# Kernel tuning notes

Hardware: AMD Instinct MI355X
Metric: run time of the kernel (lower is better)

## Reference

```python
import jax, jax.numpy as jnp
import numpy as np
import math

B, E, H, HD, P, G, N, L, FF = 16, 768, 12, 64, 16, 14, 196, 12, 3072
SQRT_E = math.sqrt(E)
SQRT_HD = math.sqrt(HD)


def cosine_norm(x):
    n = jnp.linalg.norm(x, axis=-1, keepdims=True)
    return x / jnp.maximum(n, 1e-6)


def layer_norm(x, w, b, eps=1e-6):
    m = jnp.mean(x, axis=-1, keepdims=True)
    v = jnp.var(x, axis=-1, keepdims=True)
    return (x - m) / jnp.sqrt(v + eps) * w + b


def setup_inputs() -> dict:
    key = jax.random.key(0)
    ks = jax.random.split(key, 16)
    std = 0.02
    return {
        "x": jax.random.normal(ks[0], (B, 3, 224, 224), jnp.float32),
        "patch_w": jax.random.normal(ks[1], (E, 3, P, P), jnp.float32) * std,
        "patch_b": jnp.zeros((E,), jnp.float32),
        "cls_token": jax.random.normal(ks[2], (1, 1, E), jnp.float32) * std,
        "pos_embed": jax.random.normal(ks[3], (1, N + 1, E), jnp.float32) * std,
        "Wq": jax.random.normal(ks[4], (L, E, E), jnp.float32) * std,
        "Wk": jax.random.normal(ks[5], (L, E, E), jnp.float32) * std,
        "Wv": jax.random.normal(ks[6], (L, E, E), jnp.float32) * std,
        "Wo": jax.random.normal(ks[7], (L, E, E), jnp.float32) * std,
        # Scale params stored at their torch init values (s = ones * scale)
        "s_qk": jnp.ones((L, H, HD), jnp.float32) / SQRT_E,        # scale=1/sqrt(dim)
        "Wup": jax.random.normal(ks[8], (L, FF, E), jnp.float32) * std,
        "Wgate": jax.random.normal(ks[9], (L, FF, E), jnp.float32) * std,
        "Wdown": jax.random.normal(ks[10], (L, E, FF), jnp.float32) * std,
        "s_u": jnp.ones((L, FF), jnp.float32),
        "s_v": jnp.ones((L, FF), jnp.float32),
        "alpha_A": jnp.ones((L, E), jnp.float32) / SQRT_E,         # scale=1/sqrt(dim)
        "alpha_M": jnp.ones((L, E), jnp.float32) / SQRT_E,
        "fc_w": jnp.ones((E,), jnp.float32),
        "fc_b": jnp.zeros((E,), jnp.float32),
    }


def _attention(h, wq, wk, wv, wo, s_qk):
    b, n, _ = h.shape
    q = (h @ wq.T).reshape(b, n, H, HD)
    k = (h @ wk.T).reshape(b, n, H, HD)
    v = (h @ wv.T).reshape(b, n, H, HD)
    # Scale.forward(): s * (init/scale) with init=1, scale=1/sqrt(E)
    s = s_qk * SQRT_E                                   # [H, HD]
    q = cosine_norm(q) * s
    k = cosine_norm(k) * s
    logits = jnp.einsum("bnhd,bmhd->bhnm", q, k) * SQRT_HD
    attn = jax.nn.softmax(logits, axis=-1)
    out = jnp.einsum("bhnm,bmhd->bnhd", attn, v).reshape(b, n, E)
    return out @ wo.T


def _mlp(h, wup, wgate, wdown, s_u, s_v):
    u = (h @ wup.T) * s_u
    v = (h @ wgate.T) * s_v * SQRT_E                    # mlp scale = sqrt(in_features)
    hidden = u * jax.nn.silu(v)
    return hidden @ wdown.T


def _block(h, wq, wk, wv, wo, s_qk, wup, wgate, wdown, s_u, s_v, a_A, a_M):
    # alpha Scale: init=0.05, scale=1/sqrt(E) -> effective = s * 0.05 * sqrt(E)
    aA = a_A * (0.05 * SQRT_E)
    aM = a_M * (0.05 * SQRT_E)
    h_A = cosine_norm(_attention(h, wq, wk, wv, wo, s_qk))
    h = cosine_norm(h + aA * (h_A - h))
    h_M = cosine_norm(_mlp(h, wup, wgate, wdown, s_u, s_v))
    h = cosine_norm(h + aM * (h_M - h))
    return h


def reference(x, patch_w, patch_b, cls_token, pos_embed, Wq, Wk, Wv, Wo, s_qk,
              Wup, Wgate, Wdown, s_u, s_v, alpha_A, alpha_M, fc_w, fc_b):
    b = x.shape[0]
    # patch embed: conv k=stride=16 == patch extraction + linear proj
    patches = x.reshape(b, 3, G, P, G, P).transpose(0, 2, 4, 1, 3, 5).reshape(b, N, 3 * P * P)
    t = patches @ patch_w.reshape(E, -1).T + patch_b    # [B, N, E]
    t = jnp.concatenate([jnp.broadcast_to(cls_token, (b, 1, E)), t], axis=1)
    t = t + pos_embed                                    # [B, N+1, E]
    nodes = None
    for i in range(L):
        t = _block(t, Wq[i], Wk[i], Wv[i], Wo[i], s_qk[i],
                   Wup[i], Wgate[i], Wdown[i], s_u[i], s_v[i], alpha_A[i], alpha_M[i])
        if i == L - 2:
            nodes = layer_norm(t, fc_w, fc_b)[:, 1:]
    edges = layer_norm(t, fc_w, fc_b)[:, 1:]
    return nodes, edges
```

## Files before the change

kernel.cpp:

```cpp
#include <hip/hip_runtime.h>
#include <hip/hip_bf16.h>
#include <cstdint>
#include <cstddef>

typedef __hip_bfloat16 bf16;
typedef short bf16x8 __attribute__((ext_vector_type(8)));
typedef float f32x4 __attribute__((ext_vector_type(4)));

#define SQRT_E   27.712812921102035f
#define ASCALE   (0.05f * 27.712812921102035f)
#define MPAD     3200

__device__ __forceinline__ void load_lds16(const bf16* g, bf16* l) {
    __builtin_amdgcn_global_load_lds(
        (const __attribute__((address_space(1))) void*)g,
        (__attribute__((address_space(3))) void*)l, 16, 0, 0);
}

__device__ __forceinline__ float block_sum(float v, float* sbuf) {
#pragma unroll
    for (int m = 32; m >= 1; m >>= 1) v += __shfl_xor(v, m);
    __syncthreads();
    if ((threadIdx.x & 63) == 0) sbuf[threadIdx.x >> 6] = v;
    __syncthreads();
    return sbuf[0] + sbuf[1] + sbuf[2] + sbuf[3];
}

__device__ __forceinline__ void cvt8(const float* s, bf16* d) {
    float4 f0 = *(const float4*)s;
    float4 f1 = *(const float4*)(s + 4);
    bf16 t[8];
    t[0] = __float2bfloat16(f0.x); t[1] = __float2bfloat16(f0.y);
    t[2] = __float2bfloat16(f0.z); t[3] = __float2bfloat16(f0.w);
    t[4] = __float2bfloat16(f1.x); t[5] = __float2bfloat16(f1.y);
    t[6] = __float2bfloat16(f1.z); t[7] = __float2bfloat16(f1.w);
    *reinterpret_cast<uint4*>(d) = *reinterpret_cast<const uint4*>(t);
}

__device__ __forceinline__ void wconv_body(
    int idx,
    const float* __restrict__ wq, const float* __restrict__ wk,
    const float* __restrict__ wv, const float* __restrict__ wo,
    const float* __restrict__ wu, const float* __restrict__ wg,
    const float* __restrict__ wd, bf16* __restrict__ dst) {
    const float* src;
    size_t off;
    if (idx < 294912) {
        int seg = idx / 73728, o = idx - seg * 73728;
        src = (seg == 0) ? wq : (seg == 1) ? wk : (seg == 2) ? wv : wo;
        off = (size_t)o * 8;
    } else {
        int i2 = idx - 294912;
        int seg = i2 / 294912, o = i2 - seg * 294912;
        src = (seg == 0) ? wu : (seg == 1) ? wg : wd;
        off = (size_t)o * 8;
    }
    cvt8(src + off, dst + (size_t)idx * 8);
}

__global__ __launch_bounds__(256) void prep_kernel(
    const float* __restrict__ x, bf16* __restrict__ A,
    const float* __restrict__ patchw, bf16* __restrict__ pwb,
    const float* __restrict__ wq, const float* __restrict__ wk,
    const float* __restrict__ wv, const float* __restrict__ wo,
    const float* __restrict__ wu, const float* __restrict__ wg,
    const float* __restrict__ wd, bf16* __restrict__ wdst) {
    int b = blockIdx.x, tid = threadIdx.x;
    if (b < 288) {
        int idx = b * 256 + tid;
        cvt8(patchw + (size_t)idx * 8, pwb + (size_t)idx * 8);
    } else if (b < 9888) {
        int idx = (b - 288) * 256 + tid;
        int row = idx / 768, col = idx - row * 768;
        if (row >= 3136) { A[idx] = __float2bfloat16(0.f); return; }
        int bb = row / 196, pp = row - bb * 196;
        int gy = pp / 14, gx = pp - gy * 14;
        int c = col >> 8, rem = col & 255, py = rem >> 4, px = rem & 15;
        A[idx] = __float2bfloat16(
            x[((size_t)(bb * 3 + c) * 224 + gy * 16 + py) * 224 + gx * 16 + px]);
    } else {
        int idx = (b - 9888) * 256 + tid;
        wconv_body(idx, wq, wk, wv, wo, wu, wg, wd, wdst);
    }
}

__global__ __launch_bounds__(256) void assemble_kernel(
    const float* __restrict__ tproj, const float* __restrict__ pb,
    const float* __restrict__ cls, const float* __restrict__ pos,
    float* __restrict__ h, bf16* __restrict__ hb) {
    int row = blockIdx.x;
    int b = row / 197, n = row - b * 197;
#pragma unroll
    for (int i = 0; i < 3; i++) {
        int c = threadIdx.x + i * 256;
        float v;
        if (n == 0) v = cls[c] + pos[c];
        else v = tproj[(size_t)(b * 196 + n - 1) * 768 + c] + pb[c] + pos[(size_t)n * 768 + c];
        h[(size_t)row * 768 + c] = v;
        hb[(size_t)row * 768 + c] = __float2bfloat16(v);
    }
}

__global__ __launch_bounds__(256) void gemm_bt(
    const bf16* __restrict__ A, int lda,
    const bf16* __restrict__ B0, const bf16* __restrict__ B1, const bf16* __restrict__ B2,
    int tilesPerSeg, int segColStride,
    void* __restrict__ Cv, int ldc, long long partStride,
    int Klen, int ldb, int outBf16) {
    __shared__ __align__(16) bf16 As[128 * 32];
    __shared__ __align__(16) bf16 Bs[128 * 32];
    const int tid = threadIdx.x;
    const int lane = tid & 63, wave = tid >> 6;
    const int wm = wave & 1, wn = wave >> 1;
    const int quad = lane >> 4, l16 = lane & 15;
    const int seg = blockIdx.x / tilesPerSeg;
    const int nt = blockIdx.x - seg * tilesPerSeg;
    const bf16* B = (seg == 0) ? B0 : (seg == 1 ? B1 : B2);
    const int row0 = blockIdx.y * 128;
    const int col0 = nt * 128;
    const long long kofs = (long long)blockIdx.z * Klen;
    const bf16* Ab = A + (size_t)row0 * lda + kofs;
    const bf16* Bb = B + (size_t)col0 * ldb + kofs;
    const long long cofs = (long long)blockIdx.z * partStride + (long long)seg * segColStride;

    f32x4 acc[4][4];
    f32x4 zero = {0.f, 0.f, 0.f, 0.f};
#pragma unroll
    for (int i = 0; i < 4; i++)
#pragma unroll
        for (int j = 0; j < 4; j++) acc[i][j] = zero;

    for (int k0 = 0; k0 < Klen; k0 += 32) {
#pragma unroll
        for (int it = 0; it < 2; ++it) {
            int cidx = it * 256 + tid;
            int r = cidx >> 2, cg = cidx & 3;
            load_lds16(Ab + (size_t)r * lda + k0 + cg * 8, As + cidx * 8);
            load_lds16(Bb + (size_t)r * ldb + k0 + cg * 8, Bs + cidx * 8);
        }
        __syncthreads();
        bf16x8 av[4], bv[4];
#pragma unroll
        for (int i = 0; i < 4; i++) {
            av[i] = *(const bf16x8*)(As + (wm * 64 + i * 16 + l16) * 32 + quad * 8);
            bv[i] = *(const bf16x8*)(Bs + (wn * 64 + i * 16 + l16) * 32 + quad * 8);
        }
#pragma unroll
        for (int i = 0; i < 4; i++)
#pragma unroll
            for (int j = 0; j < 4; j++)
                acc[i][j] = __builtin_amdgcn_mfma_f32_16x16x32_bf16(av[i], bv[j], acc[i][j], 0, 0, 0);
        __syncthreads();
    }
    if (outBf16) {
        bf16* Cb = (bf16*)Cv + cofs;
#pragma unroll
        for (int i = 0; i < 4; i++) {
            int rr = row0 + wm * 64 + i * 16 + quad * 4;
#pragma unroll
            for (int j = 0; j < 4; j++) {
                int cc = col0 + wn * 64 + j * 16 + l16;
#pragma unroll
                for (int r = 0; r < 4; r++)
                    Cb[(size_t)(rr + r) * ldc + cc] = __float2bfloat16(acc[i][j][r]);
            }
        }
    } else {
        float* Cb = (float*)Cv + cofs;
#pragma unroll
        for (int i = 0; i < 4; i++) {
            int rr = row0 + wm * 64 + i * 16 + quad * 4;
#pragma unroll
            for (int j = 0; j < 4; j++) {
                int cc = col0 + wn * 64 + j * 16 + l16;
#pragma unroll
                for (int r = 0; r < 4; r++)
                    Cb[(size_t)(rr + r) * ldc + cc] = acc[i][j][r];
            }
        }
    }
}

__global__ __launch_bounds__(256) void oproj_wconv(
    const bf16* __restrict__ A, const bf16* __restrict__ Bw,
    bf16* __restrict__ C, long long partStride,
    const float* __restrict__ wq, const float* __restrict__ wk,
    const float* __restrict__ wv, const float* __restrict__ wo,
    const float* __restrict__ wu, const float* __restrict__ wg,
    const float* __restrict__ wd, bf16* __restrict__ wdst) {
    __shared__ __align__(16) bf16 As[128 * 32];
    __shared__ __align__(16) bf16 Bs[128 * 32];
    const int bb = blockIdx.x;
    const int tid = threadIdx.x;
    if (bb >= 300) {
        int idx = (bb - 300) * 256 + tid;
        wconv_body(idx, wq, wk, wv, wo, wu, wg, wd, wdst);
        return;
    }
    const int lane = tid & 63, wave = tid >> 6;
    const int wm = wave & 1, wn = wave >> 1;
    const int quad = lane >> 4, l16 = lane & 15;
    const int nt = bb % 6;
    const int ry = (bb / 6) % 25;
    const int z  = bb / 150;
    const int row0 = ry * 128, col0 = nt * 128;
    const bf16* Ab = A + (size_t)row0 * 768 + z * 384;
    const bf16* Bb = Bw + (size_t)col0 * 768 + z * 384;

    f32x4 acc[4][4];
    f32x4 zero = {0.f, 0.f, 0.f, 0.f};
#pragma unroll
    for (int i = 0; i < 4; i++)
#pragma unroll
        for (int j = 0; j < 4; j++) acc[i][j] = zero;

    for (int k0 = 0; k0 < 384; k0 += 32) {
#pragma unroll
        for (int it = 0; it < 2; ++it) {
            int cidx = it * 256 + tid;
            int r = cidx >> 2, cg = cidx & 3;
            load_lds16(Ab + (size_t)r * 768 + k0 + cg * 8, As + cidx * 8);
            load_lds16(Bb + (size_t)r * 768 + k0 + cg * 8, Bs + cidx * 8);
        }
        __syncthreads();
        bf16x8 av[4], bv[4];
#pragma unroll
        for (int i = 0; i < 4; i++) {
            av[i] = *(const bf16x8*)(As + (wm * 64 + i * 16 + l16) * 32 + quad * 8);
            bv[i] = *(const bf16x8*)(Bs + (wn * 64 + i * 16 + l16) * 32 + quad * 8);
        }
#pragma unroll
        for (int i = 0; i < 4; i++)
#pragma unroll
            for (int j = 0; j < 4; j++)
                acc[i][j] = __builtin_amdgcn_mfma_f32_16x16x32_bf16(av[i], bv[j], acc[i][j], 0, 0, 0);
        __syncthreads();
    }
    bf16* Cb = C + (long long)z * partStride;
#pragma unroll
    for (int i = 0; i < 4; i++) {
        int rr = row0 + wm * 64 + i * 16 + quad * 4;
#pragma unroll
        for (int j = 0; j < 4; j++) {
            int cc = col0 + wn * 64 + j * 16 + l16;
#pragma unroll
            for (int r = 0; r < 4; r++)
                Cb[(size_t)(rr + r) * 768 + cc] = __float2bfloat16(acc[i][j][r]);
        }
    }
}

__global__ __launch_bounds__(256) void gemm_qkv(
    const bf16* __restrict__ A,
    const bf16* __restrict__ Bq, const bf16* __restrict__ Bk, const bf16* __restrict__ Bv,
    const float* __restrict__ s_l,
    bf16* __restrict__ Qd, bf16* __restrict__ Kd, bf16* __restrict__ VTd) {
    __shared__ __align__(16) bf16 As[128 * 32];
    __shared__ __align__(16) bf16 Bs[128 * 32];
    const int tid = threadIdx.x;
    const int lane = tid & 63, wave = tid >> 6;
    const int wm = wave & 1, wn = wave >> 1;
    const int quad = lane >> 4, l16 = lane & 15;
    const int seg = blockIdx.x / 6;
    const int nt = blockIdx.x - seg * 6;
    const bf16* B = (seg == 0) ? Bq : (seg == 1 ? Bk : Bv);
    const int row0 = blockIdx.y * 128;
    const int col0 = nt * 128;
    const bf16* Ab = A + (size_t)row0 * 768;
    const bf16* Bb = B + (size_t)col0 * 768;

    f32x4 acc[4][4];
    f32x4 zero = {0.f, 0.f, 0.f, 0.f};
#pragma unroll
    for (int i = 0; i < 4; i++)
#pragma unroll
        for (int j = 0; j < 4; j++) acc[i][j] = zero;

    for (int k0 = 0; k0 < 768; k0 += 32) {
#pragma unroll
        for (int it = 0; it < 2; ++it) {
            int cidx = it * 256 + tid;
            int r = cidx >> 2, cg = cidx & 3;
            load_lds16(Ab + (size_t)r * 768 + k0 + cg * 8, As + cidx * 8);
            load_lds16(Bb + (size_t)r * 768 + k0 + cg * 8, Bs + cidx * 8);
        }
        __syncthreads();
        bf16x8 av[4], bv[4];
#pragma unroll
        for (int i = 0; i < 4; i++) {
            av[i] = *(const bf16x8*)(As + (wm * 64 + i * 16 + l16) * 32 + quad * 8);
            bv[i] = *(const bf16x8*)(Bs + (wn * 64 + i * 16 + l16) * 32 + quad * 8);
        }
#pragma unroll
        for (int i = 0; i < 4; i++)
#pragma unroll
            for (int j = 0; j < 4; j++)
                acc[i][j] = __builtin_amdgcn_mfma_f32_16x16x32_bf16(av[i], bv[j], acc[i][j], 0, 0, 0);
        __syncthreads();
    }

    const int hcol = nt * 2 + wn;
    if (seg < 2) {
        bf16* Dst = (seg == 0) ? Qd : Kd;
        float sv0[4];
#pragma unroll
        for (int j = 0; j < 4; j++) sv0[j] = s_l[hcol * 64 + j * 16 + l16] * SQRT_E;
#pragma unroll
        for (int i = 0; i < 4; i++) {
#pragma unroll
            for (int r = 0; r < 4; r++) {
                float ss = acc[i][0][r] * acc[i][0][r] + acc[i][1][r] * acc[i][1][r]
                         + acc[i][2][r] * acc[i][2][r] + acc[i][3][r] * acc[i][3][r];
#pragma unroll
                for (int m = 1; m < 16; m <<= 1) ss += __shfl_xor(ss, m);
                float inv = 1.f / fmaxf(sqrtf(ss), 1e-6f);
                int t = row0 + wm * 64 + i * 16 + quad * 4 + r;
                if (t < 3152) {
                    int b = t / 197, n = t - b * 197;
                    size_t base = ((size_t)(b * 12 + hcol) * 208 + n) * 64;
#pragma unroll
                    for (int j = 0; j < 4; j++)
                        Dst[base + j * 16 + l16] =
                            __float2bfloat16(acc[i][j][r] * inv * sv0[j]);
                }
            }
        }
    } else {
#pragma unroll
        for (int i = 0; i < 4; i++) {
#pragma unroll
            for (int r = 0; r < 4; r++) {
                int t = row0 + wm * 64 + i * 16 + quad * 4 + r;
                if (t < 3152) {
                    int b = t / 197, n = t - b * 197;
                    size_t vbase = (size_t)(b * 12 + hcol) * 64 * 224 + n;
#pragma unroll
                    for (int j = 0; j < 4; j++)
                        VTd[vbase + (size_t)(j * 16 + l16) * 224] =
                            __float2bfloat16(acc[i][j][r]);
                }
            }
        }
    }
}

__global__ __launch_bounds__(256) void gemm_upgate(
    const bf16* __restrict__ A, const bf16* __restrict__ Bu, const bf16* __restrict__ Bv,
    const float* __restrict__ su, const float* __restrict__ sv,
    bf16* __restrict__ H) {
    __shared__ __align__(16) bf16 As[128 * 32];
    __shared__ __align__(16) bf16 Bus[64 * 32];
    __shared__ __align__(16) bf16 Bvs[64 * 32];
    const int tid = threadIdx.x;
    const int lane = tid & 63, wave = tid >> 6;
    const int wm = wave & 1, wn = wave >> 1;
    const int quad = lane >> 4, l16 = lane & 15;
    const int ct = blockIdx.x;
    const int row0 = blockIdx.y * 128;
    const bf16* Ab = A + (size_t)row0 * 768;
    const bf16* Bub = Bu + (size_t)ct * 64 * 768;
    const bf16* Bvb = Bv + (size_t)ct * 64 * 768;

    f32x4 au[4][2], av_[4][2];
    f32x4 zero = {0.f, 0.f, 0.f, 0.f};
#pragma unroll
    for (int i = 0; i < 4; i++)
#pragma unroll
        for (int j = 0; j < 2; j++) { au[i][j] = zero; av_[i][j] = zero; }

    for (int k0 = 0; k0 < 768; k0 += 32) {
#pragma unroll
        for (int it = 0; it < 2; ++it) {
            int cidx = it * 256 + tid;
            int r = cidx >> 2, cg = cidx & 3;
            load_lds16(Ab + (size_t)r * 768 + k0 + cg * 8, As + cidx * 8);
        }
        {
            int r = tid >> 2, cg = tid & 3;
            load_lds16(Bub + (size_t)r * 768 + k0 + cg * 8, Bus + tid * 8);
            load_lds16(Bvb + (size_t)r * 768 + k0 + cg * 8, Bvs + tid * 8);
        }
        __syncthreads();
        bf16x8 a[4], bu[2], bv[2];
#pragma unroll
        for (int i = 0; i < 4; i++)
            a[i] = *(const bf16x8*)(As + (wm * 64 + i * 16 + l16) * 32 + quad * 8);
#pragma unroll
        for (int j = 0; j < 2; j++) {
            bu[j] = *(const bf16x8*)(Bus + (wn * 32 + j * 16 + l16) * 32 + quad * 8);
            bv[j] = *(const bf16x8*)(Bvs + (wn * 32 + j * 16 + l16) * 32 + quad * 8);
        }
#pragma unroll
        for (int i = 0; i < 4; i++)
#pragma unroll
            for (int j = 0; j < 2; j++) {
                au[i][j]  = __builtin_amdgcn_mfma_f32_16x16x32_bf16(a[i], bu[j], au[i][j], 0, 0, 0);
                av_[i][j] = __builtin_amdgcn_mfma_f32_16x16x32_bf16(a[i], bv[j], av_[i][j], 0, 0, 0);
            }
        __syncthreads();
    }
#pragma unroll
    for (int j = 0; j < 2; j++) {
        int cc = ct * 64 + wn * 32 + j * 16 + l16;
        float suc = su[cc];
        float svc = sv[cc] * SQRT_E;
#pragma unroll
        for (int i = 0; i < 4; i++) {
            int rr = row0 + wm * 64 + i * 16 + quad * 4;
#pragma unroll
            for (int r = 0; r < 4; r++) {
                float u = au[i][j][r] * suc;
                float v = av_[i][j][r] * svc;
                float sig = 1.f / (1.f + __expf(-v));
                H[(size_t)(rr + r) * 3072 + cc] = __float2bfloat16(u * v * sig);
            }
        }
    }
}

__global__ __launch_bounds__(64) void attn_kernel(
    const bf16* __restrict__ Q, const bf16* __restrict__ K,
    const bf16* __restrict__ VT, bf16* __restrict__ O) {
    __shared__ __align__(16) bf16 Ps[16 * 224];
    int lane = threadIdx.x;
    int quad = lane >> 4, l16 = lane & 15;
    int bh = blockIdx.x % 192;
    int qt = blockIdx.x / 192;
    int b = bh / 12, h = bh - b * 12;
    const bf16* Qb = Q + (size_t)bh * 208 * 64;
    const bf16* Kb = K + (size_t)bh * 208 * 64;
    const bf16* Vb = VT + (size_t)bh * 64 * 224;
    f32x4 zero = {0.f, 0.f, 0.f, 0.f};

    bf16x8 a0 = *(const bf16x8*)(Qb + (qt * 16 + l16) * 64 + quad * 8);
    bf16x8 a1 = *(const bf16x8*)(Qb + (qt * 16 + l16) * 64 + quad * 8 + 32);

    f32x4 lg[13];
#pragma unroll
    for (int kt = 0; kt < 13; kt++) {
        bf16x8 b0 = *(const bf16x8*)(Kb + (kt * 16 + l16) * 64 + quad * 8);
        bf16x8 b1 = *(const bf16x8*)(Kb + (kt * 16 + l16) * 64 + quad * 8 + 32);
        f32x4 c = zero;
        c = __builtin_amdgcn_mfma_f32_16x16x32_bf16(a0, b0, c, 0, 0, 0);
        c = __builtin_amdgcn_mfma_f32_16x16x32_bf16(a1, b1, c, 0, 0, 0);
        lg[kt] = c;
    }
    float sm[4] = {0.f, 0.f, 0.f, 0.f};
#pragma unroll
    for (int kt = 0; kt < 13; kt++) {
        bool valid = (kt * 16 + l16) < 197;
#pragma unroll
        for (int r = 0; r < 4; r++) {
            float p = valid ? __expf(lg[kt][r] * 8.0f) : 0.f;
            lg[kt][r] = p;
            sm[r] += p;
        }
    }
#pragma unroll
    for (int m = 1; m < 16; m <<= 1)
#pragma unroll
        for (int r = 0; r < 4; r++) sm[r] += __shfl_xor(sm[r], m);
    float inv[4];
#pragma unroll
    for (int r = 0; r < 4; r++) inv[r] = 1.f / sm[r];
#pragma unroll
    for (int kt = 0; kt < 13; kt++)
#pragma unroll
        for (int r = 0; r < 4; r++)
            Ps[(quad * 4 + r) * 224 + kt * 16 + l16] = __float2bfloat16(lg[kt][r]);
#pragma unroll
    for (int r = 0; r < 4; r++)
        Ps[(quad * 4 + r) * 224 + 208 + l16] = __float2bfloat16(0.f);
    __syncthreads();
#pragma unroll
    for (int nt = 0; nt < 4; nt++) {
        f32x4 o = zero;
#pragma unroll
        for (int ks = 0; ks < 7; ks++) {
            bf16x8 pa = *(const bf16x8*)(Ps + l16 * 224 + ks * 32 + quad * 8);
            bf16x8 vb = *(const bf16x8*)(Vb + (nt * 16 + l16) * 224 + ks * 32 + quad * 8);
            o = __builtin_amdgcn_mfma_f32_16x16x32_bf16(pa, vb, o, 0, 0, 0);
        }
#pragma unroll
        for (int r = 0; r < 4; r++) {
            int tok = qt * 16 + quad * 4 + r;
            if (tok < 197)
                O[(size_t)(b * 197 + tok) * 768 + h * 64 + nt * 16 + l16] =
                    __float2bfloat16(o[r] * inv[r]);
        }
    }
}

__global__ __launch_bounds__(256) void residual_cos(
    const bf16* __restrict__ proj, int nParts, long long partStride,
    const float* __restrict__ alpha,
    float* __restrict__ h, bf16* __restrict__ hb,
    const float* __restrict__ fcw, const float* __restrict__ fcb,
    float* __restrict__ lnout) {
    __shared__ float sbuf[4];
    int row = blockIdx.x, tid = threadIdx.x;
    float p[3];
    float ss = 0.f;
#pragma unroll
    for (int i = 0; i < 3; i++) {
        int c = tid + i * 256;
        float v = 0.f;
        for (int pt = 0; pt < nParts; pt++)
            v += __bfloat162float(proj[(long long)pt * partStride + (size_t)row * 768 + c]);
        p[i] = v;
        ss += v * v;
    }
    ss = block_sum(ss, sbuf);
    float inv1 = 1.f / fmaxf(sqrtf(ss), 1e-6f);
    float ss2 = 0.f;
#pragma unroll
    for (int i = 0; i < 3; i++) {
        int c = tid + i * 256;
        float hv = h[(size_t)row * 768 + c];
        float a = alpha[c] * ASCALE;
        float m = hv + a * (p[i] * inv1 - hv);
        p[i] = m;
        ss2 += m * m;
    }
    ss2 = block_sum(ss2, sbuf);
    float inv2 = 1.f / fmaxf(sqrtf(ss2), 1e-6f);
    float v0 = p[0] * inv2, v1 = p[1] * inv2, v2 = p[2] * inv2;
    {
        int c = tid;
        h[(size_t)row * 768 + c] = v0;
        hb[(size_t)row * 768 + c] = __float2bfloat16(v0);
        h[(size_t)row * 768 + c + 256] = v1;
        hb[(size_t)row * 768 + c + 256] = __float2bfloat16(v1);
        h[(size_t)row * 768 + c + 512] = v2;
        hb[(size_t)row * 768 + c + 512] = __float2bfloat16(v2);
    }
    if (lnout) {
        float s = block_sum(v0 + v1 + v2, sbuf);
        float mean = s * (1.f / 768.f);
        float var = (1.f / 768.f) - mean * mean;
        float invs = 1.f / sqrtf(var + 1e-6f);
        int b = row / 197, n = row - b * 197;
        if (n >= 1) {
            size_t obase = (size_t)(b * 196 + n - 1) * 768;
            lnout[obase + tid]       = (v0 - mean) * invs * fcw[tid] + fcb[tid];
            lnout[obase + tid + 256] = (v1 - mean) * invs * fcw[tid + 256] + fcb[tid + 256];
            lnout[obase + tid + 512] = (v2 - mean) * invs * fcw[tid + 512] + fcb[tid + 512];
        }
    }
}

extern "C" void kernel_launch(void* const* d_in, const int* in_sizes, int n_in,
                              void* d_out, int out_size, void* d_ws, size_t ws_size,
                              hipStream_t stream) {
    (void)in_sizes; (void)n_in; (void)out_size; (void)ws_size;
    const float* x      = (const float*)d_in[0];
    const float* patchw = (const float*)d_in[1];
    const float* patchb = (const float*)d_in[2];
    const float* cls    = (const float*)d_in[3];
    const float* pos    = (const float*)d_in[4];
    const float* Wq     = (const float*)d_in[5];
    const float* Wk     = (const float*)d_in[6];
    const float* Wv     = (const float*)d_in[7];
    const float* Wo     = (const float*)d_in[8];
    const float* s_qk   = (const float*)d_in[9];
    const float* Wup    = (const float*)d_in[10];
    const float* Wgate  = (const float*)d_in[11];
    const float* Wdown  = (const float*)d_in[12];
    const float* s_u    = (const float*)d_in[13];
    const float* s_v    = (const float*)d_in[14];
    const float* alA    = (const float*)d_in[15];
    const float* alM    = (const float*)d_in[16];
    const float* fcw    = (const float*)d_in[17];
    const float* fcb    = (const float*)d_in[18];
    float* out = (float*)d_out;

    char* ws = (char*)d_ws;
    size_t ofs = 0;
    auto alloc = [&](size_t bytes) -> void* {
        void* p = ws + ofs;
        ofs += (bytes + 255) & ~(size_t)255;
        return p;
    };
    float* h      = (float*)alloc((size_t)MPAD * 768 * 4);
    float* part   = (float*)alloc((size_t)4 * MPAD * 768 * 4);
    bf16*  hb     = (bf16*)alloc((size_t)MPAD * 768 * 2);
    bf16*  attno  = (bf16*)alloc((size_t)MPAD * 768 * 2);
    bf16*  hidden = (bf16*)alloc((size_t)MPAD * 3072 * 2);
    size_t qkvt_bytes = ((size_t)192 * 208 * 64 * 2) * 2 + (size_t)192 * 64 * 224 * 2;
    bf16*  Qb     = (bf16*)alloc(qkvt_bytes);
    bf16*  Kb     = Qb + (size_t)192 * 208 * 64;
    bf16*  VTb    = Kb + (size_t)192 * 208 * 64;
    const size_t WPL = 9437184;
    bf16*  wbf0   = (bf16*)alloc(WPL * 2);
    bf16*  wbf1   = (bf16*)alloc(WPL * 2);
    bf16*  pwb    = (bf16*)alloc((size_t)589824 * 2);

    float* tproj  = part;
    bf16*  partb  = (bf16*)part;
    bf16*  Apatch = hidden;

    const long long PSTR = (long long)MPAD * 768;
    const size_t EE = 768 * 768, FE = (size_t)3072 * 768;

    prep_kernel<<<14496, 256, 0, stream>>>(x, Apatch, patchw, pwb,
                                           Wq, Wk, Wv, Wo, Wup, Wgate, Wdown, wbf0);
    gemm_bt<<<dim3(6, 25, 1), 256, 0, stream>>>(Apatch, 768, pwb, pwb, pwb,
                                                6, 0, tproj, 768, 0, 768, 768, 0);
    assemble_kernel<<<3152, 256, 0, stream>>>(tproj, patchb, cls, pos, h, hb);
    hipMemsetAsync(Qb, 0, qkvt_bytes, stream);

    for (int l = 0; l < 12; l++) {
        bf16* wl    = (l & 1) ? wbf1 : wbf0;
        bf16* wnext = (l & 1) ? wbf0 : wbf1;
        bf16* wqb = wl;
        bf16* wkb = wl + 589824;
        bf16* wvb = wl + 1179648;
        bf16* wob = wl + 1769472;
        bf16* wub = wl + 2359296;
        bf16* wgb = wl + 4718592;
        bf16* wdb = wl + 7077888;
        int ln = (l < 11) ? (l + 1) : l;

        gemm_qkv<<<dim3(18, 25), 256, 0, stream>>>(hb, wqb, wkb, wvb,
                                                   s_qk + (size_t)l * 768, Qb, Kb, VTb);
        attn_kernel<<<2496, 64, 0, stream>>>(Qb, Kb, VTb, attno);
        oproj_wconv<<<(l < 11) ? 4908 : 300, 256, 0, stream>>>(
            attno, wob, partb, PSTR,
            Wq + (size_t)ln * EE, Wk + (size_t)ln * EE,
            Wv + (size_t)ln * EE, Wo + (size_t)ln * EE,
            Wup + (size_t)ln * FE, Wgate + (size_t)ln * FE,
            Wdown + (size_t)ln * FE, wnext);
        residual_cos<<<3152, 256, 0, stream>>>(partb, 2, PSTR, alA + (size_t)l * 768,
                                               h, hb, fcw, fcb, (float*)nullptr);
        gemm_upgate<<<dim3(48, 25), 256, 0, stream>>>(hb, wub, wgb,
                                                      s_u + (size_t)l * 3072,
                                                      s_v + (size_t)l * 3072, hidden);
        gemm_bt<<<dim3(6, 25, 4), 256, 0, stream>>>(hidden, 3072, wdb, wdb, wdb,
                                                    6, 0, partb, 768, PSTR, 768, 3072, 1);
        float* lnp = (l == 10) ? out : (l == 11) ? (out + 2408448) : (float*)nullptr;
        residual_cos<<<3152, 256, 0, stream>>>(partb, 4, PSTR, alM + (size_t)l * 768,
                                               h, hb, fcw, fcb, lnp);
    }
}
```

Baseline: 2.370 ms.

## Fuse patch GEMM with embedding assembly and pack four attention waves per block

Merges the patch-embedding GEMM, bias/position add, CLS-row write and layer-0 weight conversion into a single kernel, dropping the separate assemble pass and the fp32 intermediate round trip. Weight conversion moves out of prep into the fused kernel's extra blocks. The attention kernel now runs four independent (batch,head) waves per 256-thread block, each with its own LDS slice, instead of one 64-thread block each. This removes a launch and intermediate traffic, but the fused epilogue does scattered per-element writes with integer division.

```diff
diff --git a/kernel.cpp b/kernel.cpp
--- a/kernel.cpp
+++ b/kernel.cpp
@@ -60,16 +60,12 @@
 
 __global__ __launch_bounds__(256) void prep_kernel(
     const float* __restrict__ x, bf16* __restrict__ A,
-    const float* __restrict__ patchw, bf16* __restrict__ pwb,
-    const float* __restrict__ wq, const float* __restrict__ wk,
-    const float* __restrict__ wv, const float* __restrict__ wo,
-    const float* __restrict__ wu, const float* __restrict__ wg,
-    const float* __restrict__ wd, bf16* __restrict__ wdst) {
+    const float* __restrict__ patchw, bf16* __restrict__ pwb) {
     int b = blockIdx.x, tid = threadIdx.x;
     if (b < 288) {
         int idx = b * 256 + tid;
         cvt8(patchw + (size_t)idx * 8, pwb + (size_t)idx * 8);
-    } else if (b < 9888) {
+    } else {
         int idx = (b - 288) * 256 + tid;
         int row = idx / 768, col = idx - row * 768;
         if (row >= 3136) { A[idx] = __float2bfloat16(0.f); return; }
@@ -78,26 +74,95 @@
         int c = col >> 8, rem = col & 255, py = rem >> 4, px = rem & 15;
         A[idx] = __float2bfloat16(
             x[((size_t)(bb * 3 + c) * 224 + gy * 16 + py) * 224 + gx * 16 + px]);
-    } else {
-        int idx = (b - 9888) * 256 + tid;
+    }
+}
+
+__global__ __launch_bounds__(256) void patch_fused(
+    const bf16* __restrict__ A, const bf16* __restrict__ Bw,
+    const float* __restrict__ pb, const float* __restrict__ cls,
+    const float* __restrict__ pos,
+    float* __restrict__ h, bf16* __restrict__ hb,
+    const float* __restrict__ wq, const float* __restrict__ wk,
+    const float* __restrict__ wv, const float* __restrict__ wo,
+    const float* __restrict__ wu, const float* __restrict__ wg,
+    const float* __restrict__ wd, bf16* __restrict__ wdst) {
+    __shared__ __align__(16) bf16 As[128 * 32];
+    __shared__ __align__(16) bf16 Bs[128 * 32];
+    const int bb = blockIdx.x;
+    const int tid = threadIdx.x;
+    if (bb >= 166) {
+        int idx = (bb - 166) * 256 + tid;
         wconv_body(idx, wq, wk, wv, wo, wu, wg, wd, wdst);
-    }
-}
-
-__global__ __launch_bounds__(256) void assemble_kernel(
-    const float* __restrict__ tproj, const float* __restrict__ pb,
-    const float* __restrict__ cls, const float* __restrict__ pos,
-    float* __restrict__ h, bf16* __restrict__ hb) {
-    int row = blockIdx.x;
-    int b = row / 197, n = row - b * 197;
-#pragma unroll
-    for (int i = 0; i < 3; i++) {
-        int c = threadIdx.x + i * 256;
-        float v;
-        if (n == 0) v = cls[c] + pos[c];
-        else v = tproj[(size_t)(b * 196 + n - 1) * 768 + c] + pb[c] + pos[(size_t)n * 768 + c];
-        h[(size_t)row * 768 + c] = v;
-        hb[(size_t)row * 768 + c] = __float2bfloat16(v);
+        return;
+    }
+    if (bb >= 150) {
+        int bi = bb - 150;
+        size_t row = (size_t)bi * 197 * 768;
+#pragma unroll
+        for (int i = 0; i < 3; i++) {
+            int c = tid + i * 256;
+            float v = cls[c] + pos[c];
+            h[row + c] = v;
+            hb[row + c] = __float2bfloat16(v);
+        }
+        return;
+    }
+    const int lane = tid & 63, wave = tid >> 6;
+    const int wm = wave & 1, wn = wave >> 1;
+    const int quad = lane >> 4, l16 = lane & 15;
+    const int nt = bb % 6;
+    const int row0 = (bb / 6) * 128;
+    const int col0 = nt * 128;
+    const bf16* Ab = A + (size_t)row0 * 768;
+    const bf16* Bb = Bw + (size_t)col0 * 768;
+
+    f32x4 acc[4][4];
+    f32x4 zero = {0.f, 0.f, 0.f, 0.f};
+#pragma unroll
+    for (int i = 0; i < 4; i++)
+#pragma unroll
+        for (int j = 0; j < 4; j++) acc[i][j] = zero;
+
+    for (int k0 = 0; k0 < 768; k0 += 32) {
+#pragma unroll
+        for (int it = 0; it < 2; ++it) {
+            int cidx = it * 256 + tid;
+            int r = cidx >> 2, cg = cidx & 3;
+            load_lds16(Ab + (size_t)r * 768 + k0 + cg * 8, As + cidx * 8);
+            load_lds16(Bb + (size_t)r * 768 + k0 + cg * 8, Bs + cidx * 8);
+        }
+        __syncthreads();
+        bf16x8 av[4], bv[4];
+#pragma unroll
+        for (int i = 0; i < 4; i++) {
+            av[i] = *(const bf16x8*)(As + (wm * 64 + i * 16 + l16) * 32 + quad * 8);
+            bv[i] = *(const bf16x8*)(Bs + (wn * 64 + i * 16 + l16) * 32 + quad * 8);
+        }
+#pragma unroll
+        for (int i = 0; i < 4; i++)
+#pragma unroll
+            for (int j = 0; j < 4; j++)
+                acc[i][j] = __builtin_amdgcn_mfma_f32_16x16x32_bf16(av[i], bv[j], acc[i][j], 0, 0, 0);
+        __syncthreads();
+    }
+#pragma unroll
+    for (int i = 0; i < 4; i++) {
+        int rr = row0 + wm * 64 + i * 16 + quad * 4;
+#pragma unroll
+        for (int j = 0; j < 4; j++) {
+            int cc = col0 + wn * 64 + j * 16 + l16;
+#pragma unroll
+            for (int r = 0; r < 4; r++) {
+                int p = rr + r;
+                if (p < 3136) {
+                    int bi = p / 196, n = p - bi * 196;
+                    float val = acc[i][j][r] + pb[cc] + pos[(size_t)(n + 1) * 768 + cc];
+                    size_t hr = (size_t)(bi * 197 + n + 1) * 768 + cc;
+                    h[hr] = val;
+                    hb[hr] = __float2bfloat16(val);
+                }
+            }
+        }
     }
 }
 
@@ -418,15 +483,17 @@
     }
 }
 
-__global__ __launch_bounds__(64) void attn_kernel(
+__global__ __launch_bounds__(256) void attn_kernel(
     const bf16* __restrict__ Q, const bf16* __restrict__ K,
     const bf16* __restrict__ VT, bf16* __restrict__ O) {
-    __shared__ __align__(16) bf16 Ps[16 * 224];
-    int lane = threadIdx.x;
+    __shared__ __align__(16) bf16 Ps[4 * 16 * 224];
+    int tid = threadIdx.x;
+    int lane = tid & 63, wave = tid >> 6;
     int quad = lane >> 4, l16 = lane & 15;
-    int bh = blockIdx.x % 192;
-    int qt = blockIdx.x / 192;
+    int qt = blockIdx.x / 48;
+    int bh = (blockIdx.x % 48) * 4 + wave;
     int b = bh / 12, h = bh - b * 12;
+    bf16* Psw = Ps + wave * (16 * 224);
     const bf16* Qb = Q + (size_t)bh * 208 * 64;
     const bf16* Kb = K + (size_t)bh * 208 * 64;
     const bf16* Vb = VT + (size_t)bh * 64 * 224;
@@ -467,17 +534,17 @@
     for (int kt = 0; kt < 13; kt++)
 #pragma unroll
         for (int r = 0; r < 4; r++)
-            Ps[(quad * 4 + r) * 224 + kt * 16 + l16] = __float2bfloat16(lg[kt][r]);
+            Psw[(quad * 4 + r) * 224 + kt * 16 + l16] = __float2bfloat16(lg[kt][r]);
 #pragma unroll
     for (int r = 0; r < 4; r++)
-        Ps[(quad * 4 + r) * 224 + 208 + l16] = __float2bfloat16(0.f);
+        Psw[(quad * 4 + r) * 224 + 208 + l16] = __float2bfloat16(0.f);
     __syncthreads();
 #pragma unroll
     for (int nt = 0; nt < 4; nt++) {
         f32x4 o = zero;
 #pragma unroll
         for (int ks = 0; ks < 7; ks++) {
-            bf16x8 pa = *(const bf16x8*)(Ps + l16 * 224 + ks * 32 + quad * 8);
+            bf16x8 pa = *(const bf16x8*)(Psw + l16 * 224 + ks * 32 + quad * 8);
             bf16x8 vb = *(const bf16x8*)(Vb + (nt * 16 + l16) * 224 + ks * 32 + quad * 8);
             o = __builtin_amdgcn_mfma_f32_16x16x32_bf16(pa, vb, o, 0, 0, 0);
         }
@@ -595,18 +662,15 @@
     bf16*  wbf1   = (bf16*)alloc(WPL * 2);
     bf16*  pwb    = (bf16*)alloc((size_t)589824 * 2);
 
-    float* tproj  = part;
     bf16*  partb  = (bf16*)part;
     bf16*  Apatch = hidden;
 
     const long long PSTR = (long long)MPAD * 768;
     const size_t EE = 768 * 768, FE = (size_t)3072 * 768;
 
-    prep_kernel<<<14496, 256, 0, stream>>>(x, Apatch, patchw, pwb,
-                                           Wq, Wk, Wv, Wo, Wup, Wgate, Wdown, wbf0);
-    gemm_bt<<<dim3(6, 25, 1), 256, 0, stream>>>(Apatch, 768, pwb, pwb, pwb,
-                                                6, 0, tproj, 768, 0, 768, 768, 0);
-    assemble_kernel<<<3152, 256, 0, stream>>>(tproj, patchb, cls, pos, h, hb);
+    prep_kernel<<<9888, 256, 0, stream>>>(x, Apatch, patchw, pwb);
+    patch_fused<<<4774, 256, 0, stream>>>(Apatch, pwb, patchb, cls, pos, h, hb,
+                                          Wq, Wk, Wv, Wo, Wup, Wgate, Wdown, wbf0);
     hipMemsetAsync(Qb, 0, qkvt_bytes, stream);
 
     for (int l = 0; l < 12; l++) {
@@ -623,7 +687,7 @@
 
         gemm_qkv<<<dim3(18, 25), 256, 0, stream>>>(hb, wqb, wkb, wvb,
                                                    s_qk + (size_t)l * 768, Qb, Kb, VTb);
-        attn_kernel<<<2496, 64, 0, stream>>>(Qb, Kb, VTb, attno);
+        attn_kernel<<<624, 256, 0, stream>>>(Qb, Kb, VTb, attno);
         oproj_wconv<<<(l < 11) ? 4908 : 300, 256, 0, stream>>>(
             attno, wob, partb, PSTR,
             Wq + (size_t)ln * EE, Wk + (size_t)ln * EE,
```

New measurement: 2.388 ms. About the same (+0.8%).

## Fuse patch GEMM with embedding assembly and move weight conversion into QKV GEMM

Applied to the files above, without the earlier changes.

Fuses the patch-embedding GEMM with the bias, cls-token and positional-embedding assembly into one kernel, dropping the separate fp32 projection buffer and the assemble launch. The first layer's weight conversion now rides on the tail blocks of that kernel. For later layers it moves from the o-projection kernel into the QKV GEMM launch, and o-proj goes back to the generic split-K gemm_bt. This saves launches and intermediate traffic, but the QKV launch grid becomes 1D and may contend with the conversion blocks.

```diff
diff --git a/kernel.cpp b/kernel.cpp
--- a/kernel.cpp
+++ b/kernel.cpp
@@ -60,16 +60,12 @@
 
 __global__ __launch_bounds__(256) void prep_kernel(
     const float* __restrict__ x, bf16* __restrict__ A,
-    const float* __restrict__ patchw, bf16* __restrict__ pwb,
-    const float* __restrict__ wq, const float* __restrict__ wk,
-    const float* __restrict__ wv, const float* __restrict__ wo,
-    const float* __restrict__ wu, const float* __restrict__ wg,
-    const float* __restrict__ wd, bf16* __restrict__ wdst) {
+    const float* __restrict__ patchw, bf16* __restrict__ pwb) {
     int b = blockIdx.x, tid = threadIdx.x;
     if (b < 288) {
         int idx = b * 256 + tid;
         cvt8(patchw + (size_t)idx * 8, pwb + (size_t)idx * 8);
-    } else if (b < 9888) {
+    } else {
         int idx = (b - 288) * 256 + tid;
         int row = idx / 768, col = idx - row * 768;
         if (row >= 3136) { A[idx] = __float2bfloat16(0.f); return; }
@@ -78,26 +74,95 @@
         int c = col >> 8, rem = col & 255, py = rem >> 4, px = rem & 15;
         A[idx] = __float2bfloat16(
             x[((size_t)(bb * 3 + c) * 224 + gy * 16 + py) * 224 + gx * 16 + px]);
-    } else {
-        int idx = (b - 9888) * 256 + tid;
+    }
+}
+
+__global__ __launch_bounds__(256) void patch_fused(
+    const bf16* __restrict__ A, const bf16* __restrict__ Bw,
+    const float* __restrict__ pb, const float* __restrict__ cls,
+    const float* __restrict__ pos,
+    float* __restrict__ h, bf16* __restrict__ hb,
+    const float* __restrict__ wq, const float* __restrict__ wk,
+    const float* __restrict__ wv, const float* __restrict__ wo,
+    const float* __restrict__ wu, const float* __restrict__ wg,
+    const float* __restrict__ wd, bf16* __restrict__ wdst) {
+    __shared__ __align__(16) bf16 As[128 * 32];
+    __shared__ __align__(16) bf16 Bs[128 * 32];
+    const int bb = blockIdx.x;
+    const int tid = threadIdx.x;
+    if (bb >= 166) {
+        int idx = (bb - 166) * 256 + tid;
         wconv_body(idx, wq, wk, wv, wo, wu, wg, wd, wdst);
-    }
-}
-
-__global__ __launch_bounds__(256) void assemble_kernel(
-    const float* __restrict__ tproj, const float* __restrict__ pb,
-    const float* __restrict__ cls, const float* __restrict__ pos,
-    float* __restrict__ h, bf16* __restrict__ hb) {
-    int row = blockIdx.x;
-    int b = row / 197, n = row - b * 197;
-#pragma unroll
-    for (int i = 0; i < 3; i++) {
-        int c = threadIdx.x + i * 256;
-        float v;
-        if (n == 0) v = cls[c] + pos[c];
-        else v = tproj[(size_t)(b * 196 + n - 1) * 768 + c] + pb[c] + pos[(size_t)n * 768 + c];
-        h[(size_t)row * 768 + c] = v;
-        hb[(size_t)row * 768 + c] = __float2bfloat16(v);
+        return;
+    }
+    if (bb >= 150) {
+        int bi = bb - 150;
+        size_t row = (size_t)bi * 197 * 768;
+#pragma unroll
+        for (int i = 0; i < 3; i++) {
+            int c = tid + i * 256;
+            float v = cls[c] + pos[c];
+            h[row + c] = v;
+            hb[row + c] = __float2bfloat16(v);
+        }
+        return;
+    }
+    const int lane = tid & 63, wave = tid >> 6;
+    const int wm = wave & 1, wn = wave >> 1;
+    const int quad = lane >> 4, l16 = lane & 15;
+    const int nt = bb % 6;
+    const int row0 = (bb / 6) * 128;
+    const int col0 = nt * 128;
+    const bf16* Ab = A + (size_t)row0 * 768;
+    const bf16* Bb = Bw + (size_t)col0 * 768;
+
+    f32x4 acc[4][4];
+    f32x4 zero = {0.f, 0.f, 0.f, 0.f};
+#pragma unroll
+    for (int i = 0; i < 4; i++)
+#pragma unroll
+        for (int j = 0; j < 4; j++) acc[i][j] = zero;
+
+    for (int k0 = 0; k0 < 768; k0 += 32) {
+#pragma unroll
+        for (int it = 0; it < 2; ++it) {
+            int cidx = it * 256 + tid;
+            int r = cidx >> 2, cg = cidx & 3;
+            load_lds16(Ab + (size_t)r * 768 + k0 + cg * 8, As + cidx * 8);
+            load_lds16(Bb + (size_t)r * 768 + k0 + cg * 8, Bs + cidx * 8);
+        }
+        __syncthreads();
+        bf16x8 av[4], bv[4];
+#pragma unroll
+        for (int i = 0; i < 4; i++) {
+            av[i] = *(const bf16x8*)(As + (wm * 64 + i * 16 + l16) * 32 + quad * 8);
+            bv[i] = *(const bf16x8*)(Bs + (wn * 64 + i * 16 + l16) * 32 + quad * 8);
+        }
+#pragma unroll
+        for (int i = 0; i < 4; i++)
+#pragma unroll
+            for (int j = 0; j < 4; j++)
+                acc[i][j] = __builtin_amdgcn_mfma_f32_16x16x32_bf16(av[i], bv[j], acc[i][j], 0, 0, 0);
+        __syncthreads();
+    }
+#pragma unroll
+    for (int i = 0; i < 4; i++) {
+        int rr = row0 + wm * 64 + i * 16 + quad * 4;
+#pragma unroll
+        for (int j = 0; j < 4; j++) {
+            int cc = col0 + wn * 64 + j * 16 + l16;
+#pragma unroll
+            for (int r = 0; r < 4; r++) {
+                int p = rr + r;
+                if (p < 3136) {
+                    int bi = p / 196, n = p - bi * 196;
+                    float val = acc[i][j][r] + pb[cc] + pos[(size_t)(n + 1) * 768 + cc];
+                    size_t hr = (size_t)(bi * 197 + n + 1) * 768 + cc;
+                    h[hr] = val;
+                    hb[hr] = __float2bfloat16(val);
+                }
+            }
+        }
     }
 }
 
@@ -181,9 +246,11 @@
     }
 }
 
-__global__ __launch_bounds__(256) void oproj_wconv(
-    const bf16* __restrict__ A, const bf16* __restrict__ Bw,
-    bf16* __restrict__ C, long long partStride,
+__global__ __launch_bounds__(256) void gemm_qkv(
+    const bf16* __restrict__ A,
+    const bf16* __restrict__ Bq, const bf16* __restrict__ Bk, const bf16* __restrict__ Bv,
+    const float* __restrict__ s_l,
+    bf16* __restrict__ Qd, bf16* __restrict__ Kd, bf16* __restrict__ VTd,
     const float* __restrict__ wq, const float* __restrict__ wk,
     const float* __restrict__ wv, const float* __restrict__ wo,
     const float* __restrict__ wu, const float* __restrict__ wg,
@@ -192,80 +259,20 @@
     __shared__ __align__(16) bf16 Bs[128 * 32];
     const int bb = blockIdx.x;
     const int tid = threadIdx.x;
-    if (bb >= 300) {
-        int idx = (bb - 300) * 256 + tid;
+    if (bb >= 450) {
+        int idx = (bb - 450) * 256 + tid;
         wconv_body(idx, wq, wk, wv, wo, wu, wg, wd, wdst);
         return;
     }
     const int lane = tid & 63, wave = tid >> 6;
     const int wm = wave & 1, wn = wave >> 1;
     const int quad = lane >> 4, l16 = lane & 15;
-    const int nt = bb % 6;
-    const int ry = (bb / 6) % 25;
-    const int z  = bb / 150;
-    const int row0 = ry * 128, col0 = nt * 128;
-    const bf16* Ab = A + (size_t)row0 * 768 + z * 384;
-    const bf16* Bb = Bw + (size_t)col0 * 768 + z * 384;
-
-    f32x4 acc[4][4];
-    f32x4 zero = {0.f, 0.f, 0.f, 0.f};
-#pragma unroll
-    for (int i = 0; i < 4; i++)
-#pragma unroll
-        for (int j = 0; j < 4; j++) acc[i][j] = zero;
-
-    for (int k0 = 0; k0 < 384; k0 += 32) {
-#pragma unroll
-        for (int it = 0; it < 2; ++it) {
-            int cidx = it * 256 + tid;
-            int r = cidx >> 2, cg = cidx & 3;
-            load_lds16(Ab + (size_t)r * 768 + k0 + cg * 8, As + cidx * 8);
-            load_lds16(Bb + (size_t)r * 768 + k0 + cg * 8, Bs + cidx * 8);
-        }
-        __syncthreads();
-        bf16x8 av[4], bv[4];
-#pragma unroll
-        for (int i = 0; i < 4; i++) {
-            av[i] = *(const bf16x8*)(As + (wm * 64 + i * 16 + l16) * 32 + quad * 8);
-            bv[i] = *(const bf16x8*)(Bs + (wn * 64 + i * 16 + l16) * 32 + quad * 8);
-        }
-#pragma unroll
-        for (int i = 0; i < 4; i++)
-#pragma unroll
-            for (int j = 0; j < 4; j++)
-                acc[i][j] = __builtin_amdgcn_mfma_f32_16x16x32_bf16(av[i], bv[j], acc[i][j], 0, 0, 0);
-        __syncthreads();
-    }
-    bf16* Cb = C + (long long)z * partStride;
-#pragma unroll
-    for (int i = 0; i < 4; i++) {
-        int rr = row0 + wm * 64 + i * 16 + quad * 4;
-#pragma unroll
-        for (int j = 0; j < 4; j++) {
-            int cc = col0 + wn * 64 + j * 16 + l16;
-#pragma unroll
-            for (int r = 0; r < 4; r++)
-                Cb[(size_t)(rr + r) * 768 + cc] = __float2bfloat16(acc[i][j][r]);
-        }
-    }
-}
-
-__global__ __launch_bounds__(256) void gemm_qkv(
-    const bf16* __restrict__ A,
-    const bf16* __restrict__ Bq, const bf16* __restrict__ Bk, const bf16* __restrict__ Bv,
-    const float* __restrict__ s_l,
-    bf16* __restrict__ Qd, bf16* __restrict__ Kd, bf16* __restrict__ VTd) {
-    __shared__ __align__(16) bf16 As[128 * 32];
-    __shared__ __align__(16) bf16 Bs[128 * 32];
-    const int tid = threadIdx.x;
-    const int lane = tid & 63, wave = tid >> 6;
-    const int wm = wave & 1, wn = wave >> 1;
-    const int quad = lane >> 4, l16 = lane & 15;
-    const int seg = blockIdx.x / 6;
-    const int nt = blockIdx.x - seg * 6;
+    const int seg = bb / 150;
+    const int rem = bb - seg * 150;
+    const int nt = rem % 6;
+    const int row0 = (rem / 6) * 128;
+    const int col0 = nt * 128;
     const bf16* B = (seg == 0) ? Bq : (seg == 1 ? Bk : Bv);
-    const int row0 = blockIdx.y * 128;
-    const int col0 = nt * 128;
     const bf16* Ab = A + (size_t)row0 * 768;
     const bf16* Bb = B + (size_t)col0 * 768;
 
@@ -595,18 +602,15 @@
     bf16*  wbf1   = (bf16*)alloc(WPL * 2);
     bf16*  pwb    = (bf16*)alloc((size_t)589824 * 2);
 
-    float* tproj  = part;
     bf16*  partb  = (bf16*)part;
     bf16*  Apatch = hidden;
 
     const long long PSTR = (long long)MPAD * 768;
     const size_t EE = 768 * 768, FE = (size_t)3072 * 768;
 
-    prep_kernel<<<14496, 256, 0, stream>>>(x, Apatch, patchw, pwb,
-                                           Wq, Wk, Wv, Wo, Wup, Wgate, Wdown, wbf0);
-    gemm_bt<<<dim3(6, 25, 1), 256, 0, stream>>>(Apatch, 768, pwb, pwb, pwb,
-                                                6, 0, tproj, 768, 0, 768, 768, 0);
-    assemble_kernel<<<3152, 256, 0, stream>>>(tproj, patchb, cls, pos, h, hb);
+    prep_kernel<<<9888, 256, 0, stream>>>(x, Apatch, patchw, pwb);
+    patch_fused<<<4774, 256, 0, stream>>>(Apatch, pwb, patchb, cls, pos, h, hb,
+                                          Wq, Wk, Wv, Wo, Wup, Wgate, Wdown, wbf0);
     hipMemsetAsync(Qb, 0, qkvt_bytes, stream);
 
     for (int l = 0; l < 12; l++) {
@@ -621,15 +625,15 @@
         bf16* wdb = wl + 7077888;
         int ln = (l < 11) ? (l + 1) : l;
 
-        gemm_qkv<<<dim3(18, 25), 256, 0, stream>>>(hb, wqb, wkb, wvb,
-                                                   s_qk + (size_t)l * 768, Qb, Kb, VTb);
-        attn_kernel<<<2496, 64, 0, stream>>>(Qb, Kb, VTb, attno);
-        oproj_wconv<<<(l < 11) ? 4908 : 300, 256, 0, stream>>>(
-            attno, wob, partb, PSTR,
+        gemm_qkv<<<(l < 11) ? 5058 : 450, 256, 0, stream>>>(
+            hb, wqb, wkb, wvb, s_qk + (size_t)l * 768, Qb, Kb, VTb,
             Wq + (size_t)ln * EE, Wk + (size_t)ln * EE,
             Wv + (size_t)ln * EE, Wo + (size_t)ln * EE,
             Wup + (size_t)ln * FE, Wgate + (size_t)ln * FE,
             Wdown + (size_t)ln * FE, wnext);
+        attn_kernel<<<2496, 64, 0, stream>>>(Qb, Kb, VTb, attno);
+        gemm_bt<<<dim3(6, 25, 2), 256, 0, stream>>>(attno, 768, wob, wob, wob,
+                                                    6, 0, partb, 768, PSTR, 384, 768, 1);
         residual_cos<<<3152, 256, 0, stream>>>(partb, 2, PSTR, alA + (size_t)l * 768,
                                                h, hb, fcw, fcb, (float*)nullptr);
         gemm_upgate<<<dim3(48, 25), 256, 0, stream>>>(hb, wub, wgb,
```

New measurement: 2.334 ms. About the same (-1.5%).
